# Kernel tuning notes

Measured on AMD Instinct MI355X. Metric: run time of the kernel, lower is better.

The kernel has to match this reference:

```python
import jax, jax.numpy as jnp
import numpy as np
from math import sqrt

D_MODEL = 1024
N_HEADS = 16
D_V = D_MODEL // N_HEADS
D_FF = 4 * D_MODEL
EPS = 1e-5


def setup_inputs() -> dict:
    key = jax.random.key(0)
    ks = jax.random.split(key, 12)
    N, L = 2, 2048
    s = 0.02
    return {
        'queries': jax.random.normal(ks[0], (N, L, D_MODEL), jnp.float32),
        'keys': jax.random.normal(ks[1], (N, L, D_MODEL), jnp.float32),
        'values': jax.random.normal(ks[2], (N, L, D_MODEL), jnp.float32),
        'mask': jnp.ones((N, 1, 1, L), jnp.int32),
        'fc_w': jax.random.normal(ks[3], (D_MODEL, D_MODEL), jnp.float32) * s,
        'fc_b': jnp.zeros((D_MODEL,), jnp.float32),
        'ln1_g': jnp.ones((D_MODEL,), jnp.float32),
        'ln1_b': jnp.zeros((D_MODEL,), jnp.float32),
        'ff_w1': jax.random.normal(ks[4], (D_MODEL, D_FF), jnp.float32) * s,
        'ff_b1': jnp.zeros((D_FF,), jnp.float32),
        'ff_w2': jax.random.normal(ks[5], (D_FF, D_MODEL), jnp.float32) * s,
        'ff_b2': jnp.zeros((D_MODEL,), jnp.float32),
        'ln2_g': jnp.ones((D_MODEL,), jnp.float32),
        'ln2_b': jnp.zeros((D_MODEL,), jnp.float32),
    }


def layer_norm(x, g, b):
    mu = jnp.mean(x, axis=-1, keepdims=True)
    var = jnp.mean(jnp.square(x - mu), axis=-1, keepdims=True)
    return (x - mu) * jax.lax.rsqrt(var + EPS) * g + b


def reference(queries, keys, values, mask, fc_w, fc_b, ln1_g, ln1_b,
              ff_w1, ff_b1, ff_w2, ff_b2, ln2_g, ln2_b):
    N, Lq, _ = queries.shape
    Lk = keys.shape[1]
    # NOTE: the original module never applies its Q/K/V linear layers; raw
    # inputs are reshaped directly into heads.
    q = queries.reshape(N, Lq, N_HEADS, D_V).transpose(0, 2, 1, 3)  # nhqd
    k = keys.reshape(N, Lk, N_HEADS, D_V)                           # nlhd
    v = values.reshape(N, Lk, N_HEADS, D_V)                         # nlhd
    energy = jnp.einsum('nhqd,nlhd->nhql', q, k)
    energy = jnp.where(mask == 0, -jnp.inf, energy)
    # original scales by sqrt(d_model), not sqrt(d_v)
    attn = jax.nn.softmax(energy / sqrt(D_MODEL), axis=-1)
    out = jnp.einsum('nhql,nlhd->nqhd', attn, v).reshape(N, Lq, D_MODEL)
    attention = out @ fc_w + fc_b
    x1 = layer_norm(attention + queries, ln1_g, ln1_b)
    fc = jax.nn.relu(x1 @ ff_w1 + ff_b1) @ ff_w2 + ff_b2
    x2 = layer_norm(fc + x1, ln2_g, ln2_b)
    return x2
```

## Files before the change

kernel.cpp:

```cpp
#include <hip/hip_runtime.h>
#include <stdint.h>

typedef unsigned short u16;
typedef __bf16 bf16x8 __attribute__((ext_vector_type(8), may_alias));
typedef float f32x4 __attribute__((ext_vector_type(4), may_alias));

typedef void __attribute__((address_space(1))) as1_void;
typedef void __attribute__((address_space(3))) as3_void;

#define MFMA16 __builtin_amdgcn_mfma_f32_16x16x32_bf16

__device__ __forceinline__ void async_copy16(const void* g, void* l) {
    __builtin_amdgcn_global_load_lds((as1_void*)g, (as3_void*)l, 16, 0, 0);
}

__device__ __forceinline__ u16 f2bf(float f) {
    union { float f; unsigned u; } c; c.f = f;
    unsigned u = c.u;
    u += 0x7fffu + ((u >> 16) & 1u);
    return (u16)(u >> 16);
}

__global__ __launch_bounds__(256) void cast_f32_bf16(
    const float* __restrict__ in, u16* __restrict__ out, int n4, float scale) {
    int i = blockIdx.x * 256 + threadIdx.x;
    if (i < n4) {
        f32x4 v = *(const f32x4*)&in[(size_t)i * 4];
        ushort4 o;
        o.x = f2bf(v[0] * scale); o.y = f2bf(v[1] * scale);
        o.z = f2bf(v[2] * scale); o.w = f2bf(v[3] * scale);
        *(ushort4*)&out[(size_t)i * 4] = o;
    }
}

__global__ __launch_bounds__(256) void transpose_cast(
    const float* __restrict__ in, u16* __restrict__ out, int R, int C) {
    __shared__ float tile[64][65];
    const float* inb = in + (size_t)blockIdx.z * R * C;
    u16* outb = out + (size_t)blockIdx.z * R * C;
    int t = threadIdx.x;
    int c0 = blockIdx.x * 64, r0 = blockIdx.y * 64;
    int tr = t >> 4, tc = (t & 15) * 4;
#pragma unroll
    for (int p = 0; p < 4; ++p) {
        int r = tr + p * 16;
        f32x4 v = *(const f32x4*)&inb[(size_t)(r0 + r) * C + c0 + tc];
        tile[r][tc] = v[0]; tile[r][tc + 1] = v[1];
        tile[r][tc + 2] = v[2]; tile[r][tc + 3] = v[3];
    }
    __syncthreads();
    int wc = t >> 4, wr = (t & 15) * 4;
#pragma unroll
    for (int p = 0; p < 4; ++p) {
        int cl = wc + p * 16;
        ushort4 o;
        o.x = f2bf(tile[wr + 0][cl]); o.y = f2bf(tile[wr + 1][cl]);
        o.z = f2bf(tile[wr + 2][cl]); o.w = f2bf(tile[wr + 3][cl]);
        *(ushort4*)&outb[(size_t)(c0 + cl) * R + r0 + wr] = o;
    }
}

__global__ __launch_bounds__(256) void flash_attn(
    const u16* __restrict__ Q, const u16* __restrict__ Kb,
    const u16* __restrict__ VT, const int* __restrict__ mask,
    u16* __restrict__ O) {
    __shared__ u16 kls[2][8192];
    __shared__ u16 vls[8192];
    __shared__ u16 pls[8][2048];

    const int bid = blockIdx.x;
    const int qt = bid & 15;
    const int h = (bid >> 4) & 15;
    const int n = bid >> 8;
    const int t = threadIdx.x;
    const int w = t >> 6, lane = t & 63;
    const int m16 = lane & 15, quad = lane >> 4;

    const size_t qrowA = (size_t)(n * 2048 + qt * 128 + w * 16 + m16);
    const size_t qrowB = qrowA + 64;
    bf16x8 qfA0 = *(const bf16x8*)&Q[qrowA * 1024 + h * 64 + quad * 8];
    bf16x8 qfA1 = *(const bf16x8*)&Q[qrowA * 1024 + h * 64 + 32 + quad * 8];
    bf16x8 qfB0 = *(const bf16x8*)&Q[qrowB * 1024 + h * 64 + quad * 8];
    bf16x8 qfB1 = *(const bf16x8*)&Q[qrowB * 1024 + h * 64 + 32 + quad * 8];

    const int* maskn = mask + n * 2048;
    int allones;
    {
        int ok = 1;
#pragma unroll
        for (int i = 0; i < 8; ++i) {
            int4 mv = *(const int4*)&maskn[lane * 32 + i * 4];
            ok &= (mv.x != 0) & (mv.y != 0) & (mv.z != 0) & (mv.w != 0);
        }
        allones = __all(ok);
    }

    f32x4 otA[4] = {}, otB[4] = {};
    f32x4 sumA = {}, sumB = {};

    const u16* Kbase = Kb + (size_t)(n * 2048) * 1024 + h * 64;
    const u16* Vbase = VT + (size_t)(n * 1024 + h * 64) * 2048;
    u16* pwA = &pls[w * 2][0];
    u16* pwB = &pls[w * 2 + 1][0];

#pragma unroll
    for (int i = 0; i < 4; ++i) {
        int e = w * 4 + i;
        async_copy16(&Kbase[(size_t)((e >> 1) * 16 + m16) * 1024 + (e & 1) * 32 + quad * 8],
                     &kls[0][e * 512]);
    }
    __syncthreads();

    for (int kt = 0; kt < 16; ++kt) {
        const u16* kcur = kls[kt & 1];
        if (kt + 1 < 16) {
            u16* knext = kls[(kt + 1) & 1];
#pragma unroll
            for (int i = 0; i < 4; ++i) {
                int e = w * 4 + i;
                async_copy16(&Kbase[(size_t)((kt + 1) * 128 + (e >> 1) * 16 + m16) * 1024 +
                                    (e & 1) * 32 + quad * 8], &knext[e * 512]);
            }
        }
#pragma unroll
        for (int i = 0; i < 4; ++i) {
            int e = w * 4 + i;
            async_copy16(&Vbase[(size_t)((e >> 2) * 16 + m16) * 2048 + kt * 128 +
                                (e & 3) * 32 + quad * 8], &vls[e * 512]);
        }

        f32x4 sA[8] = {}, sB[8] = {};
#pragma unroll
        for (int ct = 0; ct < 8; ++ct) {
            bf16x8 a0 = *(const bf16x8*)&kcur[(ct * 2 + 0) * 512 + lane * 8];
            bf16x8 a1 = *(const bf16x8*)&kcur[(ct * 2 + 1) * 512 + lane * 8];
            sA[ct] = MFMA16(a0, qfA0, sA[ct], 0, 0, 0);
            sA[ct] = MFMA16(a1, qfA1, sA[ct], 0, 0, 0);
            sB[ct] = MFMA16(a0, qfB0, sB[ct], 0, 0, 0);
            sB[ct] = MFMA16(a1, qfB1, sB[ct], 0, 0, 0);
        }

        if (allones) {
#pragma unroll
            for (int ct = 0; ct < 8; ++ct) {
                int c = ct * 2 + (quad >> 1);
                int off = m16 * 128 + (((c ^ m16) & 15) << 3) + (quad & 1) * 4;
                {
                    float p0 = __builtin_amdgcn_exp2f(sA[ct][0]);
                    float p1 = __builtin_amdgcn_exp2f(sA[ct][1]);
                    float p2 = __builtin_amdgcn_exp2f(sA[ct][2]);
                    float p3 = __builtin_amdgcn_exp2f(sA[ct][3]);
                    sumA[0] += p0; sumA[1] += p1; sumA[2] += p2; sumA[3] += p3;
                    unsigned lo = __builtin_amdgcn_perm(__float_as_uint(p1), __float_as_uint(p0), 0x07060302);
                    unsigned hi = __builtin_amdgcn_perm(__float_as_uint(p3), __float_as_uint(p2), 0x07060302);
                    *(uint2*)&pwA[off] = make_uint2(lo, hi);
                }
                {
                    float p0 = __builtin_amdgcn_exp2f(sB[ct][0]);
                    float p1 = __builtin_amdgcn_exp2f(sB[ct][1]);
                    float p2 = __builtin_amdgcn_exp2f(sB[ct][2]);
                    float p3 = __builtin_amdgcn_exp2f(sB[ct][3]);
                    sumB[0] += p0; sumB[1] += p1; sumB[2] += p2; sumB[3] += p3;
                    unsigned lo = __builtin_amdgcn_perm(__float_as_uint(p1), __float_as_uint(p0), 0x07060302);
                    unsigned hi = __builtin_amdgcn_perm(__float_as_uint(p3), __float_as_uint(p2), 0x07060302);
                    *(uint2*)&pwB[off] = make_uint2(lo, hi);
                }
            }
        } else {
#pragma unroll
            for (int ct = 0; ct < 8; ++ct) {
                const int4 mv = *(const int4*)&maskn[kt * 128 + ct * 16 + quad * 4];
                int c = ct * 2 + (quad >> 1);
                int off = m16 * 128 + (((c ^ m16) & 15) << 3) + (quad & 1) * 4;
                {
                    float p0 = __builtin_amdgcn_exp2f(sA[ct][0]) * (mv.x ? 1.f : 0.f);
                    float p1 = __builtin_amdgcn_exp2f(sA[ct][1]) * (mv.y ? 1.f : 0.f);
                    float p2 = __builtin_amdgcn_exp2f(sA[ct][2]) * (mv.z ? 1.f : 0.f);
                    float p3 = __builtin_amdgcn_exp2f(sA[ct][3]) * (mv.w ? 1.f : 0.f);
                    sumA[0] += p0; sumA[1] += p1; sumA[2] += p2; sumA[3] += p3;
                    unsigned lo = __builtin_amdgcn_perm(__float_as_uint(p1), __float_as_uint(p0), 0x07060302);
                    unsigned hi = __builtin_amdgcn_perm(__float_as_uint(p3), __float_as_uint(p2), 0x07060302);
                    *(uint2*)&pwA[off] = make_uint2(lo, hi);
                }
                {
                    float p0 = __builtin_amdgcn_exp2f(sB[ct][0]) * (mv.x ? 1.f : 0.f);
                    float p1 = __builtin_amdgcn_exp2f(sB[ct][1]) * (mv.y ? 1.f : 0.f);
                    float p2 = __builtin_amdgcn_exp2f(sB[ct][2]) * (mv.z ? 1.f : 0.f);
                    float p3 = __builtin_amdgcn_exp2f(sB[ct][3]) * (mv.w ? 1.f : 0.f);
                    sumB[0] += p0; sumB[1] += p1; sumB[2] += p2; sumB[3] += p3;
                    unsigned lo = __builtin_amdgcn_perm(__float_as_uint(p1), __float_as_uint(p0), 0x07060302);
                    unsigned hi = __builtin_amdgcn_perm(__float_as_uint(p3), __float_as_uint(p2), 0x07060302);
                    *(uint2*)&pwB[off] = make_uint2(lo, hi);
                }
            }
        }

        __syncthreads();

        bf16x8 pfA[4], pfB[4];
#pragma unroll
        for (int kc2 = 0; kc2 < 4; ++kc2) {
            int off = m16 * 128 + ((((kc2 * 4 + quad) ^ m16) & 15) << 3);
            pfA[kc2] = *(const bf16x8*)&pwA[off];
            pfB[kc2] = *(const bf16x8*)&pwB[off];
        }
#pragma unroll
        for (int kc2 = 0; kc2 < 4; ++kc2) {
#pragma unroll
            for (int dt = 0; dt < 4; ++dt) {
                bf16x8 vf = *(const bf16x8*)&vls[(dt * 4 + kc2) * 512 + lane * 8];
                otA[dt] = MFMA16(vf, pfA[kc2], otA[dt], 0, 0, 0);
                otB[dt] = MFMA16(vf, pfB[kc2], otB[dt], 0, 0, 0);
            }
        }
        __syncthreads();
    }

    float lA = (sumA[0] + sumA[1]) + (sumA[2] + sumA[3]);
    float lB = (sumB[0] + sumB[1]) + (sumB[2] + sumB[3]);
    lA += __shfl_xor(lA, 16); lA += __shfl_xor(lA, 32);
    lB += __shfl_xor(lB, 16); lB += __shfl_xor(lB, 32);
    float invA = 1.f / fmaxf(lA, 1e-30f);
    float invB = 1.f / fmaxf(lB, 1e-30f);

    const size_t obA = qrowA * 1024 + h * 64;
    const size_t obB = qrowB * 1024 + h * 64;
#pragma unroll
    for (int dt = 0; dt < 4; ++dt) {
        unsigned lo = (unsigned)f2bf(otA[dt][0] * invA) | ((unsigned)f2bf(otA[dt][1] * invA) << 16);
        unsigned hi = (unsigned)f2bf(otA[dt][2] * invA) | ((unsigned)f2bf(otA[dt][3] * invA) << 16);
        *(uint2*)&O[obA + dt * 16 + quad * 4] = make_uint2(lo, hi);
        lo = (unsigned)f2bf(otB[dt][0] * invB) | ((unsigned)f2bf(otB[dt][1] * invB) << 16);
        hi = (unsigned)f2bf(otB[dt][2] * invB) | ((unsigned)f2bf(otB[dt][3] * invB) << 16);
        *(uint2*)&O[obB + dt * 16 + quad * 4] = make_uint2(lo, hi);
    }
}

template <int BM, int BN, int RELU, int OUTBF>
__global__ __launch_bounds__(256) void gemm_bt(
    const u16* __restrict__ A, const u16* __restrict__ Bt,
    const float* __restrict__ bias, void* __restrict__ Cout,
    int M, int N, int K) {
    constexpr int MI = BM / 32;
    constexpr int NJ = BN / 32;
    __shared__ u16 sm[2][(BM + BN) * 64];
    const int lane = threadIdx.x & 63;
    const int w = threadIdx.x >> 6;
    const int m16 = lane & 15, quad = lane >> 4;
    const int nBn = N / BN;
    const int bm = blockIdx.x / nBn, bn = blockIdx.x % nBn;
    const int r2 = w >> 1, c2 = w & 1;

    const u16* Abase = A + (size_t)(bm * BM + m16) * K + quad * 8;
    const u16* Bbase = Bt + (size_t)(bn * BN + m16) * K + quad * 8;

    auto stage = [&](int buf, int k0) {
        u16* smA = &sm[buf][0];
        u16* smB = smA + BM * 64;
#pragma unroll
        for (int i = 0; i < MI; ++i) {
            int e = w * MI + i;
            async_copy16(&Abase[(size_t)((e >> 1) * 16) * K + k0 + (e & 1) * 32], &smA[e * 512]);
        }
#pragma unroll
        for (int i = 0; i < NJ; ++i) {
            int e = w * NJ + i;
            async_copy16(&Bbase[(size_t)((e >> 1) * 16) * K + k0 + (e & 1) * 32], &smB[e * 512]);
        }
    };

    f32x4 acc[MI][NJ] = {};
    const int nK = K >> 6;
    stage(0, 0);
    __syncthreads();
    for (int kt = 0; kt < nK; ++kt) {
        if (kt + 1 < nK) stage((kt + 1) & 1, (kt + 1) << 6);
        const u16* smA = &sm[kt & 1][0];
        const u16* smB = smA + BM * 64;
#pragma unroll
        for (int kc = 0; kc < 2; ++kc) {
            bf16x8 a[MI], b[NJ];
#pragma unroll
            for (int i = 0; i < MI; ++i)
                a[i] = *(const bf16x8*)&smA[((r2 * MI + i) * 2 + kc) * 512 + lane * 8];
#pragma unroll
            for (int j = 0; j < NJ; ++j)
                b[j] = *(const bf16x8*)&smB[((c2 * NJ + j) * 2 + kc) * 512 + lane * 8];
#pragma unroll
            for (int i = 0; i < MI; ++i)
#pragma unroll
                for (int j = 0; j < NJ; ++j)
                    acc[i][j] = MFMA16(a[i], b[j], acc[i][j], 0, 0, 0);
        }
        __syncthreads();
    }
    float bv[NJ];
#pragma unroll
    for (int j = 0; j < NJ; ++j)
        bv[j] = bias[bn * BN + c2 * (BN / 2) + j * 16 + m16];
#pragma unroll
    for (int i = 0; i < MI; ++i) {
        int row0 = bm * BM + r2 * (BM / 2) + i * 16 + quad * 4;
#pragma unroll
        for (int j = 0; j < NJ; ++j) {
            int col = bn * BN + c2 * (BN / 2) + j * 16 + m16;
#pragma unroll
            for (int r = 0; r < 4; ++r) {
                float v = acc[i][j][r] + bv[j];
                if (RELU) v = fmaxf(v, 0.f);
                size_t idx = (size_t)(row0 + r) * N + col;
                if (OUTBF) ((u16*)Cout)[idx] = f2bf(v);
                else ((float*)Cout)[idx] = v;
            }
        }
    }
}

__global__ __launch_bounds__(256) void ln_residual(
    const float* __restrict__ x, const float* __restrict__ res,
    const float* __restrict__ g, const float* __restrict__ b,
    float* __restrict__ out_f32, u16* __restrict__ out_bf16) {
    __shared__ float smr[8];
    int row = blockIdx.x;
    int t = threadIdx.x;
    f32x4 xv = *(const f32x4*)&x[(size_t)row * 1024 + t * 4];
    f32x4 rv = *(const f32x4*)&res[(size_t)row * 1024 + t * 4];
    xv += rv;
    float s = xv[0] + xv[1] + xv[2] + xv[3];
    float ss = xv[0] * xv[0] + xv[1] * xv[1] + xv[2] * xv[2] + xv[3] * xv[3];
#pragma unroll
    for (int d = 1; d < 64; d <<= 1) {
        s += __shfl_xor(s, d);
        ss += __shfl_xor(ss, d);
    }
    int w = t >> 6, lane = t & 63;
    if (lane == 0) { smr[w] = s; smr[4 + w] = ss; }
    __syncthreads();
    s = smr[0] + smr[1] + smr[2] + smr[3];
    ss = smr[4] + smr[5] + smr[6] + smr[7];
    float mu = s * (1.f / 1024.f);
    float var = ss * (1.f / 1024.f) - mu * mu;
    float rs = rsqrtf(var + 1e-5f);
    f32x4 gv = *(const f32x4*)&g[t * 4];
    f32x4 bv = *(const f32x4*)&b[t * 4];
    f32x4 y;
#pragma unroll
    for (int i = 0; i < 4; ++i) y[i] = (xv[i] - mu) * rs * gv[i] + bv[i];
    *(f32x4*)&out_f32[(size_t)row * 1024 + t * 4] = y;
    if (out_bf16) {
        ushort4 o;
        o.x = f2bf(y[0]); o.y = f2bf(y[1]); o.z = f2bf(y[2]); o.w = f2bf(y[3]);
        *(ushort4*)&out_bf16[(size_t)row * 1024 + t * 4] = o;
    }
}

extern "C" void kernel_launch(void* const* d_in, const int* in_sizes, int n_in,
                              void* d_out, int out_size, void* d_ws, size_t ws_size,
                              hipStream_t stream) {
    const float* q = (const float*)d_in[0];
    const float* k = (const float*)d_in[1];
    const float* v = (const float*)d_in[2];
    const int* mask = (const int*)d_in[3];
    const float* fc_b = (const float*)d_in[5];
    const float* ln1_g = (const float*)d_in[6];
    const float* ln1_b = (const float*)d_in[7];
    const float* ff_b1 = (const float*)d_in[9];
    const float* ff_b2 = (const float*)d_in[11];
    const float* ln2_g = (const float*)d_in[12];
    const float* ln2_b = (const float*)d_in[13];
    const float* fc_w = (const float*)d_in[4];
    const float* ff_w1 = (const float*)d_in[8];
    const float* ff_w2 = (const float*)d_in[10];

    char* ws = (char*)d_ws;
    const size_t MB = 1024 * 1024;
    u16* qbf = (u16*)(ws + 0);
    u16* kbf = (u16*)(ws + 8 * MB);
    u16* vT  = (u16*)(ws + 16 * MB);
    u16* ao  = (u16*)(ws + 24 * MB);
    u16* hbuf = (u16*)(ws + 0);
    u16* fcwT = (u16*)(ws + 32 * MB);
    u16* w1T  = (u16*)(ws + 34 * MB);
    u16* w2T  = (u16*)(ws + 42 * MB);
    float* attn_raw = (float*)(ws + 50 * MB);
    float* fc_raw   = (float*)(ws + 50 * MB);
    float* x1   = (float*)(ws + 66 * MB);
    u16* x1bf   = (u16*)(ws + 82 * MB);

    const float k2 = 0.03125f * 1.44269504088896340736f;

    cast_f32_bf16<<<4096, 256, 0, stream>>>(q, qbf, 1048576, k2);
    cast_f32_bf16<<<4096, 256, 0, stream>>>(k, kbf, 1048576, 1.0f);
    transpose_cast<<<dim3(16, 32, 2), 256, 0, stream>>>(v, vT, 2048, 1024);
    transpose_cast<<<dim3(16, 16, 1), 256, 0, stream>>>(fc_w, fcwT, 1024, 1024);
    transpose_cast<<<dim3(64, 16, 1), 256, 0, stream>>>(ff_w1, w1T, 1024, 4096);
    transpose_cast<<<dim3(16, 64, 1), 256, 0, stream>>>(ff_w2, w2T, 4096, 1024);

    flash_attn<<<512, 256, 0, stream>>>(qbf, kbf, vT, mask, ao);

    gemm_bt<64, 128, 0, 0><<<64 * 8, 256, 0, stream>>>(ao, fcwT, fc_b, attn_raw, 4096, 1024, 1024);
    ln_residual<<<4096, 256, 0, stream>>>(attn_raw, q, ln1_g, ln1_b, x1, x1bf);

    gemm_bt<128, 128, 1, 1><<<32 * 32, 256, 0, stream>>>(x1bf, w1T, ff_b1, hbuf, 4096, 4096, 1024);
    gemm_bt<64, 128, 0, 0><<<64 * 8, 256, 0, stream>>>(hbuf, w2T, ff_b2, fc_raw, 4096, 1024, 4096);
    ln_residual<<<4096, 256, 0, stream>>>(fc_raw, x1, ln2_g, ln2_b, (float*)d_out, (u16*)nullptr);
}
```

Measured before the change: 405.9 us.

## Stage GEMM tiles through registers with two-deep prefetch instead of direct-to-LDS copies

The bf16 GEMM kernel no longer uses global_load_lds async copies into the shared-memory double buffer. Each thread now loads tiles into a two-slot register buffer, two K-steps ahead, and writes them to LDS after the MFMA loop. A custom barrier waits only on lgkmcnt. The aim is to hide global-load latency behind more compute and drop the full vmcnt drain at each __syncthreads. In exchange it uses more VGPRs and adds explicit ds_write traffic, which could lower occupancy.

```diff
diff --git a/kernel.cpp b/kernel.cpp
--- a/kernel.cpp
+++ b/kernel.cpp
@@ -12,6 +12,10 @@
 
 __device__ __forceinline__ void async_copy16(const void* g, void* l) {
     __builtin_amdgcn_global_load_lds((as1_void*)g, (as3_void*)l, 16, 0, 0);
+}
+
+__device__ __forceinline__ void barrier_lgkm() {
+    asm volatile("s_waitcnt lgkmcnt(0)\n\ts_barrier" ::: "memory");
 }
 
 __device__ __forceinline__ u16 f2bf(float f) {
@@ -243,6 +247,7 @@
     int M, int N, int K) {
     constexpr int MI = BM / 32;
     constexpr int NJ = BN / 32;
+    constexpr int NLD = MI + NJ;
     __shared__ u16 sm[2][(BM + BN) * 64];
     const int lane = threadIdx.x & 63;
     const int w = threadIdx.x >> 6;
@@ -254,28 +259,47 @@
     const u16* Abase = A + (size_t)(bm * BM + m16) * K + quad * 8;
     const u16* Bbase = Bt + (size_t)(bn * BN + m16) * K + quad * 8;
 
-    auto stage = [&](int buf, int k0) {
+    bf16x8 ld[2][NLD];
+
+    auto gload = [&](int set, int k0) {
+#pragma unroll
+        for (int i = 0; i < MI; ++i) {
+            int e = w * MI + i;
+            ld[set][i] = *(const bf16x8*)&Abase[(size_t)((e >> 1) * 16) * K + k0 + (e & 1) * 32];
+        }
+#pragma unroll
+        for (int i = 0; i < NJ; ++i) {
+            int e = w * NJ + i;
+            ld[set][MI + i] = *(const bf16x8*)&Bbase[(size_t)((e >> 1) * 16) * K + k0 + (e & 1) * 32];
+        }
+    };
+    auto swrite = [&](int set, int buf) {
         u16* smA = &sm[buf][0];
         u16* smB = smA + BM * 64;
 #pragma unroll
         for (int i = 0; i < MI; ++i) {
             int e = w * MI + i;
-            async_copy16(&Abase[(size_t)((e >> 1) * 16) * K + k0 + (e & 1) * 32], &smA[e * 512]);
+            *(bf16x8*)&smA[e * 512 + lane * 8] = ld[set][i];
         }
 #pragma unroll
         for (int i = 0; i < NJ; ++i) {
             int e = w * NJ + i;
-            async_copy16(&Bbase[(size_t)((e >> 1) * 16) * K + k0 + (e & 1) * 32], &smB[e * 512]);
+            *(bf16x8*)&smB[e * 512 + lane * 8] = ld[set][MI + i];
         }
     };
 
     f32x4 acc[MI][NJ] = {};
     const int nK = K >> 6;
-    stage(0, 0);
-    __syncthreads();
+
+    gload(0, 0);
+    gload(1, 64);
+    swrite(0, 0);
+    barrier_lgkm();
+
     for (int kt = 0; kt < nK; ++kt) {
-        if (kt + 1 < nK) stage((kt + 1) & 1, (kt + 1) << 6);
-        const u16* smA = &sm[kt & 1][0];
+        const int cur = kt & 1;
+        if (kt + 2 < nK) gload(cur, (kt + 2) << 6);
+        const u16* smA = &sm[cur][0];
         const u16* smB = smA + BM * 64;
 #pragma unroll
         for (int kc = 0; kc < 2; ++kc) {
@@ -292,8 +316,12 @@
                 for (int j = 0; j < NJ; ++j)
                     acc[i][j] = MFMA16(a[i], b[j], acc[i][j], 0, 0, 0);
         }
-        __syncthreads();
-    }
+        if (kt + 1 < nK) {
+            swrite(cur ^ 1, cur ^ 1);
+            barrier_lgkm();
+        }
+    }
+
     float bv[NJ];
 #pragma unroll
     for (int j = 0; j < NJ; ++j)
```

Result: slower. 704.2 us (+73.5%).

## Stage GEMM tiles through registers with two-deep global prefetch

Applied to the files above, without the earlier changes.

The GEMM's async global-to-LDS copies are replaced with loads into registers that are issued two K-tiles ahead. Those registers are written into double-buffered shared memory, and each write is followed by a barrier that waits only on LDS operations. The loop is unrolled by two so global-load latency can overlap more MFMA work. In exchange the kernel needs more VGPRs for the staging registers and adds explicit LDS stores, which may lower occupancy.

```diff
diff --git a/kernel.cpp b/kernel.cpp
--- a/kernel.cpp
+++ b/kernel.cpp
@@ -12,6 +12,10 @@
 
 __device__ __forceinline__ void async_copy16(const void* g, void* l) {
     __builtin_amdgcn_global_load_lds((as1_void*)g, (as3_void*)l, 16, 0, 0);
+}
+
+__device__ __forceinline__ void barrier_lgkm() {
+    asm volatile("s_waitcnt lgkmcnt(0)\n\ts_barrier" ::: "memory");
 }
 
 __device__ __forceinline__ u16 f2bf(float f) {
@@ -243,6 +247,7 @@
     int M, int N, int K) {
     constexpr int MI = BM / 32;
     constexpr int NJ = BN / 32;
+    constexpr int NLD = MI + NJ;
     __shared__ u16 sm[2][(BM + BN) * 64];
     const int lane = threadIdx.x & 63;
     const int w = threadIdx.x >> 6;
@@ -254,46 +259,70 @@
     const u16* Abase = A + (size_t)(bm * BM + m16) * K + quad * 8;
     const u16* Bbase = Bt + (size_t)(bn * BN + m16) * K + quad * 8;
 
-    auto stage = [&](int buf, int k0) {
-        u16* smA = &sm[buf][0];
-        u16* smB = smA + BM * 64;
-#pragma unroll
-        for (int i = 0; i < MI; ++i) {
-            int e = w * MI + i;
-            async_copy16(&Abase[(size_t)((e >> 1) * 16) * K + k0 + (e & 1) * 32], &smA[e * 512]);
-        }
-#pragma unroll
-        for (int i = 0; i < NJ; ++i) {
-            int e = w * NJ + i;
-            async_copy16(&Bbase[(size_t)((e >> 1) * 16) * K + k0 + (e & 1) * 32], &smB[e * 512]);
-        }
-    };
+    bf16x8 ld0[NLD], ld1[NLD];
+
+#define GLOAD(LD, k0)                                                                   \
+    {                                                                                   \
+        _Pragma("unroll") for (int i = 0; i < MI; ++i) {                                \
+            int e = w * MI + i;                                                         \
+            LD[i] = *(const bf16x8*)&Abase[(size_t)((e >> 1) * 16) * K + (k0) + (e & 1) * 32]; \
+        }                                                                               \
+        _Pragma("unroll") for (int i = 0; i < NJ; ++i) {                                \
+            int e = w * NJ + i;                                                         \
+            LD[MI + i] = *(const bf16x8*)&Bbase[(size_t)((e >> 1) * 16) * K + (k0) + (e & 1) * 32]; \
+        }                                                                               \
+    }
+#define SWRITE(LD, buf)                                                                 \
+    {                                                                                   \
+        u16* smA_ = &sm[buf][0];                                                        \
+        u16* smB_ = smA_ + BM * 64;                                                     \
+        _Pragma("unroll") for (int i = 0; i < MI; ++i)                                  \
+            *(bf16x8*)&smA_[(w * MI + i) * 512 + lane * 8] = LD[i];                     \
+        _Pragma("unroll") for (int i = 0; i < NJ; ++i)                                  \
+            *(bf16x8*)&smB_[(w * NJ + i) * 512 + lane * 8] = LD[MI + i];                \
+    }
+#define COMPUTE(buf)                                                                    \
+    {                                                                                   \
+        const u16* smA_ = &sm[buf][0];                                                  \
+        const u16* smB_ = smA_ + BM * 64;                                               \
+        _Pragma("unroll") for (int kc = 0; kc < 2; ++kc) {                              \
+            bf16x8 a[MI], b[NJ];                                                        \
+            _Pragma("unroll") for (int i = 0; i < MI; ++i)                              \
+                a[i] = *(const bf16x8*)&smA_[((r2 * MI + i) * 2 + kc) * 512 + lane * 8];\
+            _Pragma("unroll") for (int j = 0; j < NJ; ++j)                              \
+                b[j] = *(const bf16x8*)&smB_[((c2 * NJ + j) * 2 + kc) * 512 + lane * 8];\
+            _Pragma("unroll") for (int i = 0; i < MI; ++i)                              \
+                _Pragma("unroll") for (int j = 0; j < NJ; ++j)                          \
+                    acc[i][j] = MFMA16(a[i], b[j], acc[i][j], 0, 0, 0);                 \
+        }                                                                               \
+    }
 
     f32x4 acc[MI][NJ] = {};
     const int nK = K >> 6;
-    stage(0, 0);
-    __syncthreads();
-    for (int kt = 0; kt < nK; ++kt) {
-        if (kt + 1 < nK) stage((kt + 1) & 1, (kt + 1) << 6);
-        const u16* smA = &sm[kt & 1][0];
-        const u16* smB = smA + BM * 64;
-#pragma unroll
-        for (int kc = 0; kc < 2; ++kc) {
-            bf16x8 a[MI], b[NJ];
-#pragma unroll
-            for (int i = 0; i < MI; ++i)
-                a[i] = *(const bf16x8*)&smA[((r2 * MI + i) * 2 + kc) * 512 + lane * 8];
-#pragma unroll
-            for (int j = 0; j < NJ; ++j)
-                b[j] = *(const bf16x8*)&smB[((c2 * NJ + j) * 2 + kc) * 512 + lane * 8];
-#pragma unroll
-            for (int i = 0; i < MI; ++i)
-#pragma unroll
-                for (int j = 0; j < NJ; ++j)
-                    acc[i][j] = MFMA16(a[i], b[j], acc[i][j], 0, 0, 0);
-        }
-        __syncthreads();
-    }
+
+    GLOAD(ld0, 0);
+    GLOAD(ld1, 64);
+    SWRITE(ld0, 0);
+    barrier_lgkm();
+
+    for (int kt = 0; kt < nK; kt += 2) {
+        if (kt + 2 < nK) GLOAD(ld0, (kt + 2) << 6);
+        COMPUTE(0);
+        if (kt + 1 < nK) {
+            SWRITE(ld1, 1);
+            barrier_lgkm();
+        }
+        if (kt + 3 < nK) GLOAD(ld1, (kt + 3) << 6);
+        if (kt + 1 < nK) COMPUTE(1);
+        if (kt + 2 < nK) {
+            SWRITE(ld0, 0);
+            barrier_lgkm();
+        }
+    }
+#undef GLOAD
+#undef SWRITE
+#undef COMPUTE
+
     float bv[NJ];
 #pragma unroll
     for (int j = 0; j < NJ; ++j)
```

New measurement: 441.5 us. 8.8% more time.

## Use fine-grained vmcnt waits and triple-buffered GEMM pipeline, shrink FFN1 tile

Applied to the files above, without the earlier changes.

Replaces __syncthreads in flash attention and the GEMM with inline-asm s_waitcnt vmcnt(N) plus s_barrier, so only the oldest outstanding async loads must land before each barrier. The GEMM moves from double to triple buffering with two tiles in flight, and each step now uses a single barrier. Flash attention reorders its V and next-K loads so that partial waits cover K and V separately. The FFN1 GEMM switches from 128x128 to 64x128 tiles, which doubles the block count. The hand-written vmcnt counts depend on the exact issue order and the number of loads per thread, which is fragile if the compiler reorders or splits loads. Removing the trailing barrier also risks a write-after-read race on the reused LDS buffers.

```diff
diff --git a/kernel.cpp b/kernel.cpp
--- a/kernel.cpp
+++ b/kernel.cpp
@@ -13,6 +13,11 @@
 __device__ __forceinline__ void async_copy16(const void* g, void* l) {
     __builtin_amdgcn_global_load_lds((as1_void*)g, (as3_void*)l, 16, 0, 0);
 }
+
+#define WB0() asm volatile("s_waitcnt vmcnt(0) lgkmcnt(0)\n\ts_barrier" ::: "memory")
+#define WB4() asm volatile("s_waitcnt vmcnt(4) lgkmcnt(0)\n\ts_barrier" ::: "memory")
+#define WB6() asm volatile("s_waitcnt vmcnt(6) lgkmcnt(0)\n\ts_barrier" ::: "memory")
+#define WB8() asm volatile("s_waitcnt vmcnt(8) lgkmcnt(0)\n\ts_barrier" ::: "memory")
 
 __device__ __forceinline__ u16 f2bf(float f) {
     union { float f; unsigned u; } c; c.f = f;
@@ -109,10 +114,16 @@
         async_copy16(&Kbase[(size_t)((e >> 1) * 16 + m16) * 1024 + (e & 1) * 32 + quad * 8],
                      &kls[0][e * 512]);
     }
-    __syncthreads();
 
     for (int kt = 0; kt < 16; ++kt) {
-        const u16* kcur = kls[kt & 1];
+        WB0();
+
+#pragma unroll
+        for (int i = 0; i < 4; ++i) {
+            int e = w * 4 + i;
+            async_copy16(&Vbase[(size_t)((e >> 2) * 16 + m16) * 2048 + kt * 128 +
+                                (e & 3) * 32 + quad * 8], &vls[e * 512]);
+        }
         if (kt + 1 < 16) {
             u16* knext = kls[(kt + 1) & 1];
 #pragma unroll
@@ -122,13 +133,8 @@
                                     (e & 1) * 32 + quad * 8], &knext[e * 512]);
             }
         }
-#pragma unroll
-        for (int i = 0; i < 4; ++i) {
-            int e = w * 4 + i;
-            async_copy16(&Vbase[(size_t)((e >> 2) * 16 + m16) * 2048 + kt * 128 +
-                                (e & 3) * 32 + quad * 8], &vls[e * 512]);
-        }
-
+
+        const u16* kcur = kls[kt & 1];
         f32x4 sA[8] = {}, sB[8] = {};
 #pragma unroll
         for (int ct = 0; ct < 8; ++ct) {
@@ -195,7 +201,7 @@
             }
         }
 
-        __syncthreads();
+        if (kt + 1 < 16) { WB4(); } else { WB0(); }
 
         bf16x8 pfA[4], pfB[4];
 #pragma unroll
@@ -213,7 +219,6 @@
                 otB[dt] = MFMA16(vf, pfB[kc2], otB[dt], 0, 0, 0);
             }
         }
-        __syncthreads();
     }
 
     float lA = (sumA[0] + sumA[1]) + (sumA[2] + sumA[3]);
@@ -243,7 +248,9 @@
     int M, int N, int K) {
     constexpr int MI = BM / 32;
     constexpr int NJ = BN / 32;
-    __shared__ u16 sm[2][(BM + BN) * 64];
+    constexpr int NC = MI + NJ;
+    constexpr int STG = (BM + BN) * 64;
+    __shared__ u16 sm[3 * STG];
     const int lane = threadIdx.x & 63;
     const int w = threadIdx.x >> 6;
     const int m16 = lane & 15, quad = lane >> 4;
@@ -254,8 +261,8 @@
     const u16* Abase = A + (size_t)(bm * BM + m16) * K + quad * 8;
     const u16* Bbase = Bt + (size_t)(bn * BN + m16) * K + quad * 8;
 
-    auto stage = [&](int buf, int k0) {
-        u16* smA = &sm[buf][0];
+    auto issue_tile = [&](int stage, int k0) {
+        u16* smA = &sm[stage * STG];
         u16* smB = smA + BM * 64;
 #pragma unroll
         for (int i = 0; i < MI; ++i) {
@@ -271,11 +278,22 @@
 
     f32x4 acc[MI][NJ] = {};
     const int nK = K >> 6;
-    stage(0, 0);
-    __syncthreads();
+
+    issue_tile(0, 0);
+    issue_tile(1, 64);
+
+    int cur = 0;
     for (int kt = 0; kt < nK; ++kt) {
-        if (kt + 1 < nK) stage((kt + 1) & 1, (kt + 1) << 6);
-        const u16* smA = &sm[kt & 1][0];
+        if (kt + 1 < nK) {
+            if constexpr (NC == 6) { WB6(); } else { WB8(); }
+        } else {
+            WB0();
+        }
+        if (kt + 2 < nK) {
+            int nxt = cur + 2; if (nxt >= 3) nxt -= 3;
+            issue_tile(nxt, (kt + 2) << 6);
+        }
+        const u16* smA = &sm[cur * STG];
         const u16* smB = smA + BM * 64;
 #pragma unroll
         for (int kc = 0; kc < 2; ++kc) {
@@ -292,8 +310,9 @@
                 for (int j = 0; j < NJ; ++j)
                     acc[i][j] = MFMA16(a[i], b[j], acc[i][j], 0, 0, 0);
         }
-        __syncthreads();
-    }
+        cur = (cur == 2) ? 0 : cur + 1;
+    }
+
     float bv[NJ];
 #pragma unroll
     for (int j = 0; j < NJ; ++j)
@@ -401,7 +420,7 @@
     gemm_bt<64, 128, 0, 0><<<64 * 8, 256, 0, stream>>>(ao, fcwT, fc_b, attn_raw, 4096, 1024, 1024);
     ln_residual<<<4096, 256, 0, stream>>>(attn_raw, q, ln1_g, ln1_b, x1, x1bf);
 
-    gemm_bt<128, 128, 1, 1><<<32 * 32, 256, 0, stream>>>(x1bf, w1T, ff_b1, hbuf, 4096, 4096, 1024);
+    gemm_bt<64, 128, 1, 1><<<64 * 32, 256, 0, stream>>>(x1bf, w1T, ff_b1, hbuf, 4096, 4096, 1024);
     gemm_bt<64, 128, 0, 0><<<64 * 8, 256, 0, stream>>>(hbuf, w2T, ff_b2, fc_raw, 4096, 1024, 4096);
     ln_residual<<<4096, 256, 0, stream>>>(fc_raw, x1, ln2_g, ln2_b, (float*)d_out, (u16*)nullptr);
 }
```

After: 431.3 us. 6.3% more time.
